# Performance work log

Hardware: AMD Instinct MI355X
Metric: run time of the kernel (lower is better)

## Reference

```python
import jax, jax.numpy as jnp
import numpy as np

B, S, D, H, V, N_SHARDS, CAP = 4, 512, 512, 8, 32000, 64, 128
HD = D // H


def _layernorm(x, g, b, eps=1e-5):
    mu = x.mean(-1, keepdims=True)
    var = ((x - mu) ** 2).mean(-1, keepdims=True)
    return (x - mu) * jax.lax.rsqrt(var + eps) * g + b


def setup_inputs() -> dict:
    key = jax.random.key(0)
    ks = jax.random.split(key, 16)
    s = 0.02
    return {
        'input_ids': jax.random.randint(ks[0], (B, S), 0, V, dtype=jnp.int32),
        'emb': jax.random.normal(ks[1], (V, D), jnp.float32) * s,
        'Wq': jax.random.normal(ks[2], (D, D), jnp.float32) * s,
        'Wk': jax.random.normal(ks[3], (D, D), jnp.float32) * s,
        'Wv': jax.random.normal(ks[4], (D, D), jnp.float32) * s,
        'Wo': jax.random.normal(ks[5], (D, D), jnp.float32) * s,
        'ln_g': jnp.ones((D,), jnp.float32),
        'ln_b': jnp.zeros((D,), jnp.float32),
        'W_router': jax.random.normal(ks[6], (D, N_SHARDS), jnp.float32),
        'mem_keys': jax.random.normal(ks[7], (N_SHARDS, CAP, D), jnp.float32) * s,
        'mem_values': jax.random.normal(ks[8], (N_SHARDS, CAP, D), jnp.float32) * s,
        'Wg_c': jax.random.normal(ks[9], (D, D), jnp.float32) * s,
        'Wg_m': jax.random.normal(ks[10], (D, D), jnp.float32) * s,
        'bg': jnp.zeros((D,), jnp.float32),
        'Wd': jax.random.normal(ks[11], (D, V), jnp.float32) * s,
        'bd': jnp.zeros((V,), jnp.float32),
        'top_k': 4,
    }


def reference(input_ids, emb, Wq, Wk, Wv, Wo, ln_g, ln_b, W_router,
              mem_keys, mem_values, Wg_c, Wg_m, bg, Wd, bd, top_k):
    # --- encode_context: embedding + causal MHA block (ContextSynthesizer) ---
    x = emb[input_ids]                                   # [B,S,D]
    q = (x @ Wq).reshape(B, S, H, HD)
    k = (x @ Wk).reshape(B, S, H, HD)
    v = (x @ Wv).reshape(B, S, H, HD)
    att = jnp.einsum('bqhd,bkhd->bhqk', q, k) / jnp.sqrt(jnp.float32(HD))
    causal = jnp.tril(jnp.ones((S, S), bool))
    att = jnp.where(causal[None, None], att, jnp.finfo(att.dtype).min)
    att = jax.nn.softmax(att, axis=-1)
    o = jnp.einsum('bhqk,bkhd->bqhd', att, v).reshape(B, S, D) @ Wo
    ctx = _layernorm(x + o, ln_g, ln_b)                  # [B,S,D]

    # --- LSHRouter: hyperplane projection -> shard id per token ---
    routes = jnp.argmax(ctx @ W_router, axis=-1)         # [B,S] int

    # --- MemoryShardStore.query, batched: per-token routed shard top-k read ---
    keys_g = mem_keys[routes]                            # [B,S,CAP,D] irregular gather
    scores = jnp.einsum('bscd,bsd->bsc', keys_g, ctx)    # [B,S,CAP]
    top_v, top_i = jax.lax.top_k(scores, top_k)          # [B,S,k]
    w = jax.nn.softmax(top_v, axis=-1)
    vals = mem_values[routes[:, :, None], top_i]         # [B,S,k,D]
    memory_stream = jnp.einsum('bsk,bskd->bsd', w, vals)

    # --- GatedMemoryFusion ---
    gate = jax.nn.sigmoid(ctx @ Wg_c + memory_stream @ Wg_m + bg)
    fused = gate * ctx + (1.0 - gate) * memory_stream

    # --- decoder; payload bias is zero (store holds no sequence_chunk records) ---
    logits = fused @ Wd + bd                             # [B,S,V]
    return logits
```

## Files before the change

### kernel.cpp

```cpp
#include <hip/hip_runtime.h>

typedef unsigned short u16;
typedef float f32x4 __attribute__((ext_vector_type(4)));
typedef short short8 __attribute__((ext_vector_type(8)));
typedef __bf16 bf16x8 __attribute__((ext_vector_type(8)));

#define B_  4
#define S_  512
#define D_  512
#define H_  8
#define HD_ 64
#define V_  32000
#define NSHARD_ 64
#define CAP_ 128
#define TOK_ (B_ * S_)

__device__ __forceinline__ float bf2f(u16 u) { return __uint_as_float(((unsigned)u) << 16); }
__device__ __forceinline__ u16 f2bf(float f) {
  unsigned u = __float_as_uint(f);
  u += 0x7FFFu + ((u >> 16) & 1u);
  return (u16)(u >> 16);
}

__device__ __forceinline__ f32x4 mfma16(short8 a, short8 b, f32x4 c) {
  return __builtin_amdgcn_mfma_f32_16x16x32_bf16(
      __builtin_bit_cast(bf16x8, a), __builtin_bit_cast(bf16x8, b), c, 0, 0, 0);
}

__device__ __forceinline__ void load_lds16(const void* g, void* l) {
  __builtin_amdgcn_global_load_lds(
      (const __attribute__((address_space(1))) void*)g,
      (__attribute__((address_space(3))) void*)l, 16, 0, 0);
}

template<int NS, bool ACC, int OM, bool CKLIM>
__global__ __launch_bounds__(256) void gemm_bt(
    const u16* __restrict__ Ah, const u16* __restrict__ Al, int ldA, long sA1, long sA2,
    const u16* __restrict__ Bh, const u16* __restrict__ Bl, int ldB, long sB1, long sB2,
    void* __restrict__ C0, void* __restrict__ C1, int ldC, long sC1, long sC2,
    int K, int z2n, float alpha)
{
  __shared__ u16 AsH[64 * 64];
  __shared__ u16 BsH[64 * 64];
  __shared__ u16 AsL[(NS == 3) ? 64 * 64 : 8];
  __shared__ u16 BsL[(NS == 3) ? 64 * 64 : 8];

  const int n0 = blockIdx.x * 64;
  const int m0 = blockIdx.y * 64;

  const int z = blockIdx.z;
  const int z1 = z / z2n, z2 = z - z1 * z2n;
  const long baseA = (long)z1 * sA1 + (long)z2 * sA2;
  const long baseB = (long)z1 * sB1 + (long)z2 * sB2;
  const long baseC = (long)z1 * sC1 + (long)z2 * sC2;

  const int tid = threadIdx.x;
  const int lane = tid & 63;
  const int w = tid >> 6;
  const int wm = (w >> 1) * 32, wn = (w & 1) * 32;
  const int fr = lane & 15, kg = lane >> 4;

  const int srow = lane >> 3;
  const int schunk = (lane & 7) ^ srow;

  const u16* gAh = Ah + baseA + (long)(m0 + w * 16 + srow) * ldA + schunk * 8;
  const u16* gBh = Bh + baseB + (long)(n0 + w * 16 + srow) * ldB + schunk * 8;
  const u16* gAl = (NS == 3) ? (Al + baseA + (long)(m0 + w * 16 + srow) * ldA + schunk * 8) : nullptr;
  const u16* gBl = (NS == 3) ? (Bl + baseB + (long)(n0 + w * 16 + srow) * ldB + schunk * 8) : nullptr;
  u16* lAh = &AsH[(w * 16) * 64];
  u16* lBh = &BsH[(w * 16) * 64];
  u16* lAl = &AsL[(NS == 3) ? (w * 16) * 64 : 0];
  u16* lBl = &BsL[(NS == 3) ? (w * 16) * 64 : 0];

  const int kmax = CKLIM ? (m0 + 64) : K;

  f32x4 acc[2][2] = {};

  for (int k0 = 0; k0 < kmax; k0 += 64) {
    load_lds16(gAh + k0, lAh);
    load_lds16(gAh + k0 + 8 * ldA, lAh + 8 * 64);
    load_lds16(gBh + k0, lBh);
    load_lds16(gBh + k0 + 8 * ldB, lBh + 8 * 64);
    if (NS == 3) {
      load_lds16(gAl + k0, lAl);
      load_lds16(gAl + k0 + 8 * ldA, lAl + 8 * 64);
      load_lds16(gBl + k0, lBl);
      load_lds16(gBl + k0 + 8 * ldB, lBl + 8 * 64);
    }
    __syncthreads();

    short8 ah[2][2], bh[2][2], al[2][2], bl[2][2];
#pragma unroll
    for (int mi = 0; mi < 2; ++mi) {
      int row = wm + mi * 16 + fr;
#pragma unroll
      for (int ks = 0; ks < 2; ++ks) {
        int idx = row * 64 + ((ks * 32 + kg * 8) ^ ((fr & 7) << 3));
        ah[mi][ks] = *(const short8*)&AsH[idx];
        if (NS == 3) al[mi][ks] = *(const short8*)&AsL[idx];
      }
    }
#pragma unroll
    for (int ni = 0; ni < 2; ++ni) {
      int row = wn + ni * 16 + fr;
#pragma unroll
      for (int ks = 0; ks < 2; ++ks) {
        int idx = row * 64 + ((ks * 32 + kg * 8) ^ ((fr & 7) << 3));
        bh[ni][ks] = *(const short8*)&BsH[idx];
        if (NS == 3) bl[ni][ks] = *(const short8*)&BsL[idx];
      }
    }
#pragma unroll
    for (int ks = 0; ks < 2; ++ks)
#pragma unroll
      for (int mi = 0; mi < 2; ++mi)
#pragma unroll
        for (int ni = 0; ni < 2; ++ni) {
          acc[mi][ni] = mfma16(ah[mi][ks], bh[ni][ks], acc[mi][ni]);
          if (NS == 3) {
            acc[mi][ni] = mfma16(ah[mi][ks], bl[ni][ks], acc[mi][ni]);
            acc[mi][ni] = mfma16(al[mi][ks], bh[ni][ks], acc[mi][ni]);
          }
        }
    __syncthreads();
  }

#pragma unroll
  for (int mi = 0; mi < 2; ++mi)
#pragma unroll
    for (int ni = 0; ni < 2; ++ni) {
      int gnc = n0 + wn + ni * 16 + fr;
#pragma unroll
      for (int r = 0; r < 4; ++r) {
        int gm = m0 + wm + mi * 16 + kg * 4 + r;
        float v = acc[mi][ni][r] * alpha;
        long idx = baseC + (long)gm * ldC + gnc;
        if (OM == 0) {
          float* C = (float*)C0;
          C[idx] = ACC ? (C[idx] + v) : v;
        } else {
          u16 h = f2bf(v);
          ((u16*)C0)[idx] = h;
          ((u16*)C1)[idx] = f2bf(v - bf2f(h));
        }
      }
    }
}

__global__ __launch_bounds__(256) void qkt_k(
    const u16* __restrict__ qkvh, const u16* __restrict__ qkvl,
    float* __restrict__ att)
{
  const int n0 = blockIdx.x * 64;
  const int m0 = blockIdx.y * 64;
  if (n0 > m0 + 63) return;
  const int z = blockIdx.z;
  const int b = z >> 3, h = z & 7;
  const long qbase = (long)b * 512 * 1536 + h * 64;
  const long kbase = qbase + 512;
  const long cbase = (long)z * 512 * 512;

  const int tid = threadIdx.x;
  const int lane = tid & 63;
  const int w = tid >> 6;
  const int wm = (w >> 1) * 32, wn = (w & 1) * 32;
  const int fr = lane & 15, kg = lane >> 4;

  short8 ah[2][2], al[2][2], bh[2][2], bl[2][2];
#pragma unroll
  for (int mi = 0; mi < 2; ++mi)
#pragma unroll
    for (int ks = 0; ks < 2; ++ks) {
      long ra = qbase + (long)(m0 + wm + mi * 16 + fr) * 1536 + ks * 32 + kg * 8;
      ah[mi][ks] = *(const short8*)(qkvh + ra);
      al[mi][ks] = *(const short8*)(qkvl + ra);
    }
#pragma unroll
  for (int ni = 0; ni < 2; ++ni)
#pragma unroll
    for (int ks = 0; ks < 2; ++ks) {
      long rb = kbase + (long)(n0 + wn + ni * 16 + fr) * 1536 + ks * 32 + kg * 8;
      bh[ni][ks] = *(const short8*)(qkvh + rb);
      bl[ni][ks] = *(const short8*)(qkvl + rb);
    }

  f32x4 acc[2][2] = {};
#pragma unroll
  for (int ks = 0; ks < 2; ++ks)
#pragma unroll
    for (int mi = 0; mi < 2; ++mi)
#pragma unroll
      for (int ni = 0; ni < 2; ++ni) {
        acc[mi][ni] = mfma16(ah[mi][ks], bh[ni][ks], acc[mi][ni]);
        acc[mi][ni] = mfma16(ah[mi][ks], bl[ni][ks], acc[mi][ni]);
        acc[mi][ni] = mfma16(al[mi][ks], bh[ni][ks], acc[mi][ni]);
      }

#pragma unroll
  for (int mi = 0; mi < 2; ++mi)
#pragma unroll
    for (int ni = 0; ni < 2; ++ni) {
      int gnc = n0 + wn + ni * 16 + fr;
#pragma unroll
      for (int r = 0; r < 4; ++r) {
        int gm = m0 + wm + mi * 16 + kg * 4 + r;
        att[cbase + (long)gm * 512 + gnc] = acc[mi][ni][r] * 0.125f;
      }
    }
}

__global__ __launch_bounds__(512, 2) void logits_gemm256_k(
    const u16* __restrict__ A, const u16* __restrict__ Bt,
    const float* __restrict__ bias, float* __restrict__ C)
{
  __shared__ u16 As[2][256 * 64];
  __shared__ u16 Bs[2][256 * 64];

  const int id = blockIdx.x;
  const int swz = (id & 7) * 125 + (id >> 3);
  const int n0 = (swz >> 3) * 256;
  const int m0 = (swz & 7) * 256;

  const int tid = threadIdx.x;
  const int lane = tid & 63;
  const int wid = tid >> 6;
  const int wr = wid >> 2, wc = wid & 3;
  const int fr = lane & 15, kg = lane >> 4;
  const int srow = lane >> 3;
  const int schunk = (lane & 7) ^ srow;

  f32x4 acc[8][4] = {};
  short8 pa0[4][2], pa1[4][2], pb0[2][2], pb1[2][2];

  auto stageA = [&](int kt, int h) {
#pragma unroll
    for (int j = 0; j < 2; ++j) {
      int r0 = j * 128 + h * 64 + wid * 8;
      load_lds16(A + (long)(m0 + r0 + srow) * D_ + kt * 64 + schunk * 8,
                 &As[kt & 1][r0 * 64]);
    }
  };
  auto stageB = [&](int kt, int h) {
#pragma unroll
    for (int j = 0; j < 2; ++j) {
      int r0 = (j * 2 + (wid >> 2)) * 64 + h * 32 + (wid & 3) * 8;
      load_lds16(Bt + (long)(n0 + r0 + srow) * D_ + kt * 64 + schunk * 8,
                 &Bs[kt & 1][r0 * 64]);
    }
  };
  auto readA = [&](short8 (&d)[4][2], int buf, int h) {
#pragma unroll
    for (int mi = 0; mi < 4; ++mi)
#pragma unroll
      for (int ks = 0; ks < 2; ++ks) {
        int row = wr * 128 + h * 64 + mi * 16 + fr;
        d[mi][ks] = *(const short8*)&As[buf][row * 64 +
                        ((ks * 32 + kg * 8) ^ ((fr & 7) << 3))];
      }
  };
  auto readB = [&](short8 (&d)[2][2], int buf, int h) {
#pragma unroll
    for (int ni = 0; ni < 2; ++ni)
#pragma unroll
      for (int ks = 0; ks < 2; ++ks) {
        int row = wc * 64 + h * 32 + ni * 16 + fr;
        d[ni][ks] = *(const short8*)&Bs[buf][row * 64 +
                        ((ks * 32 + kg * 8) ^ ((fr & 7) << 3))];
      }
  };
  auto quad = [&](short8 (&a)[4][2], short8 (&b)[2][2], int mb, int nb) {
#pragma unroll
    for (int ks = 0; ks < 2; ++ks)
#pragma unroll
      for (int mi = 0; mi < 4; ++mi)
#pragma unroll
        for (int ni = 0; ni < 2; ++ni)
          acc[mb + mi][nb + ni] = mfma16(a[mi][ks], b[ni][ks], acc[mb + mi][nb + ni]);
  };

#define SYNC_PRE()                                          \
  __builtin_amdgcn_sched_barrier(0);                        \
  __builtin_amdgcn_s_barrier();                             \
  asm volatile("s_waitcnt lgkmcnt(0)" ::: "memory");        \
  __builtin_amdgcn_sched_barrier(0);                        \
  __builtin_amdgcn_s_setprio(1);
#define SYNC_POST()                                         \
  __builtin_amdgcn_s_setprio(0);                            \
  __builtin_amdgcn_sched_barrier(0);                        \
  __builtin_amdgcn_s_barrier();                             \
  __builtin_amdgcn_sched_barrier(0);

  stageA(0, 0); stageB(0, 0); stageB(0, 1); stageA(0, 1);
  stageA(1, 0); stageB(1, 0); stageB(1, 1);
  __builtin_amdgcn_sched_barrier(0);
  asm volatile("s_waitcnt vmcnt(6)" ::: "memory");
  __builtin_amdgcn_s_barrier();
  __builtin_amdgcn_sched_barrier(0);

  for (int i = 0; i < 4; ++i) {
    const int t1 = 2 * i + 1, t2 = 2 * i + 2, t3 = 2 * i + 3;
    const bool st2 = (t2 < 8), st3 = (t3 < 8);

    readA(pa0, 0, 0); readB(pb0, 0, 0);
    stageA(t1, 1);
    SYNC_PRE(); quad(pa0, pb0, 0, 0); SYNC_POST();

    readB(pb1, 0, 1);
    if (st2) stageA(t2, 0);
    SYNC_PRE(); quad(pa0, pb1, 0, 2); SYNC_POST();

    readA(pa1, 0, 1);
    if (st2) stageB(t2, 0);
    SYNC_PRE(); quad(pa1, pb1, 4, 2); SYNC_POST();

    if (st2) stageB(t2, 1);
    __builtin_amdgcn_sched_barrier(0);
    if (st2) { asm volatile("s_waitcnt vmcnt(6)" ::: "memory"); }
    else     { asm volatile("s_waitcnt vmcnt(0)" ::: "memory"); }
    __builtin_amdgcn_s_barrier();
    __builtin_amdgcn_sched_barrier(0);
    __builtin_amdgcn_s_setprio(1);
    quad(pa1, pb0, 4, 0);
    SYNC_POST();

    readA(pa0, 1, 0); readB(pb0, 1, 0);
    if (st2) stageA(t2, 1);
    SYNC_PRE(); quad(pa0, pb0, 0, 0); SYNC_POST();

    readB(pb1, 1, 1);
    if (st3) stageA(t3, 0);
    SYNC_PRE(); quad(pa0, pb1, 0, 2); SYNC_POST();

    readA(pa1, 1, 1);
    if (st3) stageB(t3, 0);
    SYNC_PRE(); quad(pa1, pb1, 4, 2); SYNC_POST();

    if (st3) stageB(t3, 1);
    __builtin_amdgcn_sched_barrier(0);
    if (st3) { asm volatile("s_waitcnt vmcnt(6)" ::: "memory"); }
    else     { asm volatile("s_waitcnt vmcnt(0)" ::: "memory"); }
    __builtin_amdgcn_s_barrier();
    __builtin_amdgcn_sched_barrier(0);
    __builtin_amdgcn_s_setprio(1);
    quad(pa1, pb0, 4, 0);
    SYNC_POST();
  }
#undef SYNC_PRE
#undef SYNC_POST

#pragma unroll
  for (int ni = 0; ni < 4; ++ni) {
    int gnc = n0 + wc * 64 + ni * 16 + fr;
    float bv = bias[gnc];
#pragma unroll
    for (int mi = 0; mi < 8; ++mi)
#pragma unroll
      for (int r = 0; r < 4; ++r) {
        int gm = m0 + wr * 128 + mi * 16 + kg * 4 + r;
        __builtin_nontemporal_store(acc[mi][ni][r] + bv, &C[(long)gm * V_ + gnc]);
      }
  }
}

template<bool LO>
__global__ __launch_bounds__(256) void transpose_split_k(
    const float* __restrict__ W, int ldw, int ldo, int koff,
    u16* __restrict__ oh, u16* __restrict__ ol)
{
  __shared__ float t[64][65];
  const int n0 = blockIdx.x * 64;
  const int k0 = blockIdx.y * 64;
  const int tid = threadIdx.x;
  {
    const int kk = tid >> 4;
    const int c4 = (tid & 15) * 4;
#pragma unroll
    for (int i = 0; i < 4; ++i) {
      f32x4 v = *(const f32x4*)(W + (long)(k0 + kk + i * 16) * ldw + n0 + c4);
      t[kk + i * 16][c4] = v[0];
      t[kk + i * 16][c4 + 1] = v[1];
      t[kk + i * 16][c4 + 2] = v[2];
      t[kk + i * 16][c4 + 3] = v[3];
    }
  }
  __syncthreads();
  {
    const int chunk = tid & 7;
    const int nn = tid >> 3;
#pragma unroll
    for (int j = 0; j < 2; ++j) {
      int n = nn + j * 32;
      u16 hbuf[8], lbuf[8];
#pragma unroll
      for (int e = 0; e < 8; ++e) {
        float fv = t[chunk * 8 + e][n];
        u16 h = f2bf(fv);
        hbuf[e] = h;
        if (LO) lbuf[e] = f2bf(fv - bf2f(h));
      }
      long ob = (long)(n0 + n) * ldo + koff + k0 + chunk * 8;
      *(short8*)(oh + ob) = *(short8*)hbuf;
      if (LO) *(short8*)(ol + ob) = *(short8*)lbuf;
    }
  }
}

__global__ __launch_bounds__(256) void v_transpose_k(
    const u16* __restrict__ qh, const u16* __restrict__ ql,
    u16* __restrict__ vTh, u16* __restrict__ vTl)
{
  __shared__ u16 th[64][68];
  __shared__ u16 tl[64][68];
  const int z = blockIdx.y;
  const int b = z >> 3, h = z & 7;
  const int s0 = blockIdx.x * 64;
  const long ibase = ((long)(b * 512 + s0)) * 1536 + 1024 + h * 64;
  const int tid = threadIdx.x;
  {
    const int sr = tid >> 2;
    const int c8 = (tid & 3) * 16;
    const long src = ibase + (long)sr * 1536 + c8;
    *(short8*)&th[sr][c8]     = *(const short8*)(qh + src);
    *(short8*)&th[sr][c8 + 8] = *(const short8*)(qh + src + 8);
    *(short8*)&tl[sr][c8]     = *(const short8*)(ql + src);
    *(short8*)&tl[sr][c8 + 8] = *(const short8*)(ql + src + 8);
  }
  __syncthreads();
  {
    const int dr = tid >> 2;
    const int s8 = (tid & 3) * 16;
    u16 oh[16], ol[16];
#pragma unroll
    for (int j = 0; j < 16; ++j) { oh[j] = th[s8 + j][dr]; ol[j] = tl[s8 + j][dr]; }
    long ob = (long)z * 64 * 512 + (long)dr * 512 + s0 + s8;
    *(short8*)(vTh + ob)     = *(short8*)&oh[0];
    *(short8*)(vTh + ob + 8) = *(short8*)&oh[8];
    *(short8*)(vTl + ob)     = *(short8*)&ol[0];
    *(short8*)(vTl + ob + 8) = *(short8*)&ol[8];
  }
}

__global__ __launch_bounds__(128) void embed_k(const int* __restrict__ ids,
                                               const float* __restrict__ emb,
                                               float* __restrict__ x,
                                               u16* __restrict__ xh,
                                               u16* __restrict__ xl) {
  const int t = blockIdx.x;
  const long id = ids[t];
  const int c = threadIdx.x * 4;
  f32x4 v = *(const f32x4*)(emb + id * (long)D_ + c);
  *(f32x4*)(x + (long)t * D_ + c) = v;
  u16 hh[4], ll[4];
#pragma unroll
  for (int j = 0; j < 4; ++j) {
    u16 h = f2bf(v[j]);
    hh[j] = h;
    ll[j] = f2bf(v[j] - bf2f(h));
  }
  *(unsigned long long*)(xh + (long)t * D_ + c) = *(unsigned long long*)hh;
  *(unsigned long long*)(xl + (long)t * D_ + c) = *(unsigned long long*)ll;
}

__global__ __launch_bounds__(64) void softmax_causal_k(
    const float* __restrict__ att, u16* __restrict__ ph, u16* __restrict__ pl) {
  const int row = blockIdx.x;
  const int i = row & 511;
  const long base = (long)row << 9;
  const float* p = att + base;
  const int lane = threadIdx.x;
  const int c0 = lane * 8;
  float v[8];
  float m = -3.4e38f;
  if (c0 <= i) {
    f32x4 a = *(const f32x4*)(p + c0);
    f32x4 b2 = *(const f32x4*)(p + c0 + 4);
#pragma unroll
    for (int j = 0; j < 8; ++j) {
      float x = (j < 4) ? a[j] : b2[j - 4];
      x = (c0 + j <= i) ? x : -3.4e38f;
      v[j] = x;
      m = fmaxf(m, x);
    }
  } else {
#pragma unroll
    for (int j = 0; j < 8; ++j) v[j] = 0.f;
  }
#pragma unroll
  for (int off = 32; off; off >>= 1) m = fmaxf(m, __shfl_xor(m, off));
  float s = 0.f;
  if (c0 <= i) {
#pragma unroll
    for (int j = 0; j < 8; ++j) {
      float e = (c0 + j <= i) ? expf(v[j] - m) : 0.f;
      v[j] = e;
      s += e;
    }
  }
#pragma unroll
  for (int off = 32; off; off >>= 1) s += __shfl_xor(s, off);
  float inv = 1.f / s;
  if (c0 <= (i | 63)) {
    u16 hh[8], ll[8];
#pragma unroll
    for (int j = 0; j < 8; ++j) {
      float e = (c0 <= i) ? v[j] * inv : 0.f;
      u16 h = f2bf(e);
      hh[j] = h;
      ll[j] = f2bf(e - bf2f(h));
    }
    *(short8*)(ph + base + c0) = *(short8*)hh;
    *(short8*)(pl + base + c0) = *(short8*)ll;
  }
}

__global__ __launch_bounds__(256) void resid_ln_k(
    const float* __restrict__ x, const float* __restrict__ proj,
    const float* __restrict__ g, const float* __restrict__ b,
    float* __restrict__ ctxf, u16* __restrict__ catA)
{
  const int t = blockIdx.x;
  const int tid = threadIdx.x;
  __shared__ float red[8];
  const float* xr = x + (long)t * D_;
  const float* pr = proj + (long)t * D_;
  float v0 = xr[tid] + pr[tid];
  float v1 = xr[tid + 256] + pr[tid + 256];
  float s = v0 + v1, q = v0 * v0 + v1 * v1;
#pragma unroll
  for (int off = 32; off; off >>= 1) { s += __shfl_xor(s, off); q += __shfl_xor(q, off); }
  const int wave = tid >> 6, lane = tid & 63;
  if (lane == 0) { red[wave] = s; red[4 + wave] = q; }
  __syncthreads();
  s = red[0] + red[1] + red[2] + red[3];
  q = red[4] + red[5] + red[6] + red[7];
  float mu = s * (1.f / 512.f);
  float var = q * (1.f / 512.f) - mu * mu;
  float rs = rsqrtf(var + 1e-5f);
  float o0 = (v0 - mu) * rs * g[tid] + b[tid];
  float o1 = (v1 - mu) * rs * g[tid + 256] + b[tid + 256];
  long base = (long)t * D_;
  ctxf[base + tid] = o0;
  ctxf[base + tid + 256] = o1;
  long cb = (long)t * 1024;
  catA[cb + tid] = f2bf(o0);
  catA[cb + tid + 256] = f2bf(o1);
}

__global__ __launch_bounds__(128) void route_mem_k(
    const float* __restrict__ ctxf, const float* __restrict__ Wr,
    const float* __restrict__ keys, const float* __restrict__ valsm,
    float* __restrict__ msf, u16* __restrict__ catA)
{
  const int t = blockIdx.x;
  const int tid = threadIdx.x;
  __shared__ float sctx[D_];
  __shared__ float spart[CAP_];
  __shared__ float sred2[2][64];
  __shared__ int s_route;
  __shared__ int sidx[4];
  __shared__ float sw[4];

  f32x4 cv = ((const f32x4*)(ctxf + (long)t * D_))[tid];
  ((f32x4*)sctx)[tid] = cv;
  __syncthreads();

  {
    const int c = tid & 63, half = tid >> 6;
    float accr = 0.f;
    const float* cp = sctx + half * 256;
    const float* wp = Wr + (long)(half * 256) * NSHARD_ + c;
    for (int d = 0; d < 256; ++d) accr += cp[d] * wp[(long)d * NSHARD_];
    sred2[half][c] = accr;
  }
  __syncthreads();
  if (tid < 64) {
    float v = sred2[0][tid] + sred2[1][tid];
    int idx = tid;
#pragma unroll
    for (int off = 32; off; off >>= 1) {
      float ov = __shfl_xor(v, off);
      int oi = __shfl_xor(idx, off);
      if (ov > v || (ov == v && oi < idx)) { v = ov; idx = oi; }
    }
    if (tid == 0) s_route = idx;
  }
  __syncthreads();
  const int route = s_route;

  {
    const float* krow = keys + ((long)route * CAP_ + tid) * D_;
    float sc = 0.f;
    for (int d0 = 0; d0 < D_; d0 += 4) {
      f32x4 kv = *(const f32x4*)(krow + d0);
      sc += sctx[d0] * kv[0] + sctx[d0 + 1] * kv[1] +
            sctx[d0 + 2] * kv[2] + sctx[d0 + 3] * kv[3];
    }
    spart[tid] = sc;
  }
  __syncthreads();

  for (int rep = 0; rep < 4; ++rep) {
    if (tid < 64) {
      float v1 = spart[tid]; int i1 = tid;
      float v2 = spart[tid + 64]; int i2 = tid + 64;
      float v; int idx;
      if (v2 > v1) { v = v2; idx = i2; } else { v = v1; idx = i1; }
#pragma unroll
      for (int off = 32; off; off >>= 1) {
        float ov = __shfl_xor(v, off);
        int oi = __shfl_xor(idx, off);
        if (ov > v || (ov == v && oi < idx)) { v = ov; idx = oi; }
      }
      if (tid == 0) { sidx[rep] = idx; sw[rep] = v; spart[idx] = -3.4e38f; }
    }
    __syncthreads();
  }

  float w0 = sw[0], w1 = sw[1], w2 = sw[2], w3 = sw[3];
  float mx = fmaxf(fmaxf(w0, w1), fmaxf(w2, w3));
  float e0 = expf(w0 - mx), e1 = expf(w1 - mx), e2 = expf(w2 - mx), e3 = expf(w3 - mx);
  float inv = 1.f / (e0 + e1 + e2 + e3);
  float wk[4] = {e0 * inv, e1 * inv, e2 * inv, e3 * inv};

  float a0 = 0, a1 = 0, a2 = 0, a3 = 0;
#pragma unroll
  for (int k = 0; k < 4; ++k) {
    const float* vr = valsm + ((long)route * CAP_ + sidx[k]) * D_ + tid * 4;
    f32x4 vv = *(const f32x4*)vr;
    float w = wk[k];
    a0 += w * vv[0]; a1 += w * vv[1]; a2 += w * vv[2]; a3 += w * vv[3];
  }
  f32x4 of; of[0] = a0; of[1] = a1; of[2] = a2; of[3] = a3;
  *(f32x4*)(msf + (long)t * D_ + tid * 4) = of;
  u16 oh[4];
  oh[0] = f2bf(a0); oh[1] = f2bf(a1); oh[2] = f2bf(a2); oh[3] = f2bf(a3);
  *(unsigned long long*)(catA + (long)t * 1024 + 512 + tid * 4) =
      *(unsigned long long*)oh;
}

__global__ __launch_bounds__(256) void gate_fuse_k(
    const float* __restrict__ g1, const float* __restrict__ bg,
    const float* __restrict__ ctxf, const float* __restrict__ msf,
    u16* __restrict__ fused)
{
  long base = ((long)blockIdx.x * 256 + threadIdx.x) * 4;
  f32x4 gv = *(const f32x4*)(g1 + base);
  f32x4 cv = *(const f32x4*)(ctxf + base);
  f32x4 mv = *(const f32x4*)(msf + base);
  int col = (int)(base & 511);
  u16 o[4];
#pragma unroll
  for (int j = 0; j < 4; ++j) {
    float g = 1.f / (1.f + expf(-(gv[j] + bg[col + j])));
    o[j] = f2bf(g * cv[j] + (1.f - g) * mv[j]);
  }
  *(unsigned long long*)(fused + base) = *(unsigned long long*)o;
}

extern "C" void kernel_launch(void* const* d_in, const int* in_sizes, int n_in,
                              void* d_out, int out_size, void* d_ws, size_t ws_size,
                              hipStream_t stream) {
  const int*   ids  = (const int*)d_in[0];
  const float* emb  = (const float*)d_in[1];
  const float* Wq   = (const float*)d_in[2];
  const float* Wk   = (const float*)d_in[3];
  const float* Wv   = (const float*)d_in[4];
  const float* Wo   = (const float*)d_in[5];
  const float* ln_g = (const float*)d_in[6];
  const float* ln_b = (const float*)d_in[7];
  const float* Wr   = (const float*)d_in[8];
  const float* mk   = (const float*)d_in[9];
  const float* mv   = (const float*)d_in[10];
  const float* Wgc  = (const float*)d_in[11];
  const float* Wgm  = (const float*)d_in[12];
  const float* bg   = (const float*)d_in[13];
  const float* Wd   = (const float*)d_in[14];
  const float* bd   = (const float*)d_in[15];
  float* out = (float*)d_out;

  char* ws = (char*)d_ws;
  size_t off = 0;
  auto alloc = [&](size_t bytes) -> void* {
    void* p = ws + off;
    off += (bytes + 255) & ~(size_t)255;
    return p;
  };
  float* x      = (float*)alloc((size_t)TOK_ * D_ * 4);
  u16*   xh     = (u16*)  alloc((size_t)TOK_ * D_ * 2);
  u16*   xl     = (u16*)  alloc((size_t)TOK_ * D_ * 2);
  u16*   wqkvTh = (u16*)  alloc((size_t)3 * D_ * D_ * 2);
  u16*   wqkvTl = (u16*)  alloc((size_t)3 * D_ * D_ * 2);
  u16*   woTh   = (u16*)  alloc((size_t)D_ * D_ * 2);
  u16*   woTl   = (u16*)  alloc((size_t)D_ * D_ * 2);
  u16*   wgT    = (u16*)  alloc((size_t)D_ * 1024 * 2);
  u16*   wdT    = (u16*)  alloc((size_t)D_ * V_ * 2);
  u16*   qkvh   = (u16*)  alloc((size_t)TOK_ * 3 * D_ * 2);
  u16*   qkvl   = (u16*)  alloc((size_t)TOK_ * 3 * D_ * 2);
  u16*   vTh    = (u16*)  alloc((size_t)B_ * H_ * HD_ * S_ * 2);
  u16*   vTl    = (u16*)  alloc((size_t)B_ * H_ * HD_ * S_ * 2);
  float* att    = (float*)alloc((size_t)B_ * H_ * S_ * S_ * 4);
  u16*   ph     = (u16*)  alloc((size_t)B_ * H_ * S_ * S_ * 2);
  u16*   pl     = (u16*)  alloc((size_t)B_ * H_ * S_ * S_ * 2);
  u16*   oh     = (u16*)  alloc((size_t)TOK_ * D_ * 2);
  u16*   ol     = (u16*)  alloc((size_t)TOK_ * D_ * 2);
  float* proj   = (float*)alloc((size_t)TOK_ * D_ * 4);
  float* ctxf   = (float*)alloc((size_t)TOK_ * D_ * 4);
  u16*   catA   = (u16*)  alloc((size_t)TOK_ * 1024 * 2);
  float* msf    = (float*)alloc((size_t)TOK_ * D_ * 4);
  float* g1     = (float*)alloc((size_t)TOK_ * D_ * 4);
  u16*   fused  = (u16*)  alloc((size_t)TOK_ * D_ * 2);

  {
    dim3 g8(D_ / 64, D_ / 64, 1);
    transpose_split_k<true><<<g8, 256, 0, stream>>>(Wq, D_, 512, 0, wqkvTh, wqkvTl);
    transpose_split_k<true><<<g8, 256, 0, stream>>>(Wk, D_, 512, 0, wqkvTh + D_ * D_, wqkvTl + D_ * D_);
    transpose_split_k<true><<<g8, 256, 0, stream>>>(Wv, D_, 512, 0, wqkvTh + 2 * D_ * D_, wqkvTl + 2 * D_ * D_);
    transpose_split_k<true><<<g8, 256, 0, stream>>>(Wo, D_, 512, 0, woTh, woTl);
    transpose_split_k<false><<<g8, 256, 0, stream>>>(Wgc, D_, 1024, 0, wgT, nullptr);
    transpose_split_k<false><<<g8, 256, 0, stream>>>(Wgm, D_, 1024, 512, wgT, nullptr);
    dim3 gd(V_ / 64, D_ / 64, 1);
    transpose_split_k<false><<<gd, 256, 0, stream>>>(Wd, V_, 512, 0, wdT, nullptr);
  }

  embed_k<<<TOK_, 128, 0, stream>>>(ids, emb, x, xh, xl);

  {
    dim3 g(1536 / 64, TOK_ / 64, 1);
    gemm_bt<3, false, 1, false><<<g, 256, 0, stream>>>(
        xh, xl, D_, 0, 0, wqkvTh, wqkvTl, D_, 0, 0,
        qkvh, qkvl, 1536, 0, 0, D_, 1, 1.f);
  }

  {
    dim3 g(S_ / 64, B_ * H_, 1);
    v_transpose_k<<<g, 256, 0, stream>>>(qkvh, qkvl, vTh, vTl);
  }

  {
    dim3 g(S_ / 64, S_ / 64, B_ * H_);
    qkt_k<<<g, 256, 0, stream>>>(qkvh, qkvl, att);
  }

  softmax_causal_k<<<B_ * H_ * S_, 64, 0, stream>>>(att, ph, pl);

  {
    dim3 g(1, S_ / 64, B_ * H_);
    gemm_bt<3, false, 1, true><<<g, 256, 0, stream>>>(
        ph, pl, S_, (long)H_ * S_ * S_, (long)S_ * S_,
        vTh, vTl, S_, (long)H_ * HD_ * S_, (long)HD_ * S_,
        oh, ol, D_, (long)S_ * D_, HD_,
        S_, H_, 1.f);
  }

  {
    dim3 g(D_ / 64, TOK_ / 64, 1);
    gemm_bt<3, false, 0, false><<<g, 256, 0, stream>>>(
        oh, ol, D_, 0, 0, woTh, woTl, D_, 0, 0,
        proj, nullptr, D_, 0, 0, D_, 1, 1.f);
  }

  resid_ln_k<<<TOK_, 256, 0, stream>>>(x, proj, ln_g, ln_b, ctxf, catA);

  route_mem_k<<<TOK_, 128, 0, stream>>>(ctxf, Wr, mk, mv, msf, catA);

  {
    dim3 g(D_ / 64, TOK_ / 64, 1);
    gemm_bt<1, false, 0, false><<<g, 256, 0, stream>>>(
        catA, nullptr, 1024, 0, 0, wgT, nullptr, 1024, 0, 0,
        g1, nullptr, D_, 0, 0, 1024, 1, 1.f);
  }

  gate_fuse_k<<<(TOK_ * D_) / (256 * 4), 256, 0, stream>>>(g1, bg, ctxf, msf, fused);

  logits_gemm256_k<<<1000, 512, 0, stream>>>(fused, wdT, bd, out);
}
```

Measured before the change: 322.1 us.

## Rewrite logits GEMM with 256x128 tiles, BK=32 and simpler double buffering

Replaces the 256x256-tile, BK=64 logits GEMM and its fine-grained quad-interleaved schedule with a 256x128 tile over 16 K-steps of 32. Each step loads all fragments and issues a 4x4 MFMA block. The grid doubles to 2000 blocks, and the smaller LDS and register footprint targets 4 blocks per CU for more occupancy and more tiles to fill the CUs. In exchange it loses operand reuse per tile, adds more barriers per K, and drops the overlap of LDS reads with MFMA.

Measured after the change: 322.4 us. No clear change (+0.1%).

```diff
diff --git a/kernel.cpp b/kernel.cpp
--- a/kernel.cpp
+++ b/kernel.cpp
@@ -209,154 +209,91 @@
     }
 }
 
-__global__ __launch_bounds__(512, 2) void logits_gemm256_k(
+__global__ __launch_bounds__(512, 4) void logits_gemm_bk32_k(
     const u16* __restrict__ A, const u16* __restrict__ Bt,
     const float* __restrict__ bias, float* __restrict__ C)
 {
-  __shared__ u16 As[2][256 * 64];
-  __shared__ u16 Bs[2][256 * 64];
+  __shared__ u16 As[2][256 * 32];
+  __shared__ u16 Bs[2][128 * 32];
 
   const int id = blockIdx.x;
-  const int swz = (id & 7) * 125 + (id >> 3);
-  const int n0 = (swz >> 3) * 256;
+  const int swz = (id & 7) * 250 + (id >> 3);
   const int m0 = (swz & 7) * 256;
+  const int n0 = (swz >> 3) * 128;
 
   const int tid = threadIdx.x;
   const int lane = tid & 63;
   const int wid = tid >> 6;
-  const int wr = wid >> 2, wc = wid & 3;
+  const int wr = wid >> 1;
+  const int wc = wid & 1;
   const int fr = lane & 15, kg = lane >> 4;
-  const int srow = lane >> 3;
-  const int schunk = (lane & 7) ^ srow;
-
-  f32x4 acc[8][4] = {};
-  short8 pa0[4][2], pa1[4][2], pb0[2][2], pb1[2][2];
-
-  auto stageA = [&](int kt, int h) {
-#pragma unroll
-    for (int j = 0; j < 2; ++j) {
-      int r0 = j * 128 + h * 64 + wid * 8;
-      load_lds16(A + (long)(m0 + r0 + srow) * D_ + kt * 64 + schunk * 8,
-                 &As[kt & 1][r0 * 64]);
-    }
+  const int srow = lane >> 2;
+  const int schunk = (lane & 3) ^ (srow & 3);
+
+  f32x4 acc[4][4] = {};
+  short8 a[4], b[4];
+
+  auto stage = [&](int kt) {
+    const int buf = kt & 1;
+    const long kc = (long)kt * 32 + schunk * 8;
+    load_lds16(A + (long)(m0 + wid * 16 + srow) * D_ + kc,
+               &As[buf][(wid * 16) * 32]);
+    load_lds16(A + (long)(m0 + 128 + wid * 16 + srow) * D_ + kc,
+               &As[buf][(128 + wid * 16) * 32]);
+    load_lds16(Bt + (long)(n0 + wid * 16 + srow) * D_ + kc,
+               &Bs[buf][(wid * 16) * 32]);
   };
-  auto stageB = [&](int kt, int h) {
-#pragma unroll
-    for (int j = 0; j < 2; ++j) {
-      int r0 = (j * 2 + (wid >> 2)) * 64 + h * 32 + (wid & 3) * 8;
-      load_lds16(Bt + (long)(n0 + r0 + srow) * D_ + kt * 64 + schunk * 8,
-                 &Bs[kt & 1][r0 * 64]);
+  auto readfrags = [&](int buf) {
+#pragma unroll
+    for (int mi = 0; mi < 4; ++mi) {
+      int row = wr * 64 + mi * 16 + fr;
+      a[mi] = *(const short8*)&As[buf][row * 32 + ((kg ^ (row & 3)) * 8)];
+    }
+#pragma unroll
+    for (int ni = 0; ni < 4; ++ni) {
+      int row = wc * 64 + ni * 16 + fr;
+      b[ni] = *(const short8*)&Bs[buf][row * 32 + ((kg ^ (row & 3)) * 8)];
     }
   };
-  auto readA = [&](short8 (&d)[4][2], int buf, int h) {
-#pragma unroll
-    for (int mi = 0; mi < 4; ++mi)
-#pragma unroll
-      for (int ks = 0; ks < 2; ++ks) {
-        int row = wr * 128 + h * 64 + mi * 16 + fr;
-        d[mi][ks] = *(const short8*)&As[buf][row * 64 +
-                        ((ks * 32 + kg * 8) ^ ((fr & 7) << 3))];
-      }
-  };
-  auto readB = [&](short8 (&d)[2][2], int buf, int h) {
-#pragma unroll
-    for (int ni = 0; ni < 2; ++ni)
-#pragma unroll
-      for (int ks = 0; ks < 2; ++ks) {
-        int row = wc * 64 + h * 32 + ni * 16 + fr;
-        d[ni][ks] = *(const short8*)&Bs[buf][row * 64 +
-                        ((ks * 32 + kg * 8) ^ ((fr & 7) << 3))];
-      }
-  };
-  auto quad = [&](short8 (&a)[4][2], short8 (&b)[2][2], int mb, int nb) {
-#pragma unroll
-    for (int ks = 0; ks < 2; ++ks)
-#pragma unroll
-      for (int mi = 0; mi < 4; ++mi)
-#pragma unroll
-        for (int ni = 0; ni < 2; ++ni)
-          acc[mb + mi][nb + ni] = mfma16(a[mi][ks], b[ni][ks], acc[mb + mi][nb + ni]);
-  };
-
-#define SYNC_PRE()                                          \
-  __builtin_amdgcn_sched_barrier(0);                        \
-  __builtin_amdgcn_s_barrier();                             \
-  asm volatile("s_waitcnt lgkmcnt(0)" ::: "memory");        \
-  __builtin_amdgcn_sched_barrier(0);                        \
-  __builtin_amdgcn_s_setprio(1);
-#define SYNC_POST()                                         \
-  __builtin_amdgcn_s_setprio(0);                            \
-  __builtin_amdgcn_sched_barrier(0);                        \
-  __builtin_amdgcn_s_barrier();                             \
-  __builtin_amdgcn_sched_barrier(0);
-
-  stageA(0, 0); stageB(0, 0); stageB(0, 1); stageA(0, 1);
-  stageA(1, 0); stageB(1, 0); stageB(1, 1);
-  __builtin_amdgcn_sched_barrier(0);
-  asm volatile("s_waitcnt vmcnt(6)" ::: "memory");
-  __builtin_amdgcn_s_barrier();
-  __builtin_amdgcn_sched_barrier(0);
-
-  for (int i = 0; i < 4; ++i) {
-    const int t1 = 2 * i + 1, t2 = 2 * i + 2, t3 = 2 * i + 3;
-    const bool st2 = (t2 < 8), st3 = (t3 < 8);
-
-    readA(pa0, 0, 0); readB(pb0, 0, 0);
-    stageA(t1, 1);
-    SYNC_PRE(); quad(pa0, pb0, 0, 0); SYNC_POST();
-
-    readB(pb1, 0, 1);
-    if (st2) stageA(t2, 0);
-    SYNC_PRE(); quad(pa0, pb1, 0, 2); SYNC_POST();
-
-    readA(pa1, 0, 1);
-    if (st2) stageB(t2, 0);
-    SYNC_PRE(); quad(pa1, pb1, 4, 2); SYNC_POST();
-
-    if (st2) stageB(t2, 1);
+
+  stage(0);
+  stage(1);
+
+  for (int t = 0; t < 16; ++t) {
     __builtin_amdgcn_sched_barrier(0);
-    if (st2) { asm volatile("s_waitcnt vmcnt(6)" ::: "memory"); }
-    else     { asm volatile("s_waitcnt vmcnt(0)" ::: "memory"); }
+    if (t < 15) { asm volatile("s_waitcnt vmcnt(3)" ::: "memory"); }
+    else        { asm volatile("s_waitcnt vmcnt(0)" ::: "memory"); }
     __builtin_amdgcn_s_barrier();
     __builtin_amdgcn_sched_barrier(0);
-    __builtin_amdgcn_s_setprio(1);
-    quad(pa1, pb0, 4, 0);
-    SYNC_POST();
-
-    readA(pa0, 1, 0); readB(pb0, 1, 0);
-    if (st2) stageA(t2, 1);
-    SYNC_PRE(); quad(pa0, pb0, 0, 0); SYNC_POST();
-
-    readB(pb1, 1, 1);
-    if (st3) stageA(t3, 0);
-    SYNC_PRE(); quad(pa0, pb1, 0, 2); SYNC_POST();
-
-    readA(pa1, 1, 1);
-    if (st3) stageB(t3, 0);
-    SYNC_PRE(); quad(pa1, pb1, 4, 2); SYNC_POST();
-
-    if (st3) stageB(t3, 1);
+
+    readfrags(t & 1);
+    asm volatile("s_waitcnt lgkmcnt(0)" ::: "memory");
     __builtin_amdgcn_sched_barrier(0);
-    if (st3) { asm volatile("s_waitcnt vmcnt(6)" ::: "memory"); }
-    else     { asm volatile("s_waitcnt vmcnt(0)" ::: "memory"); }
     __builtin_amdgcn_s_barrier();
     __builtin_amdgcn_sched_barrier(0);
+
+    if (t + 2 < 16) stage(t + 2);
+
+    __builtin_amdgcn_sched_barrier(0);
     __builtin_amdgcn_s_setprio(1);
-    quad(pa1, pb0, 4, 0);
-    SYNC_POST();
-  }
-#undef SYNC_PRE
-#undef SYNC_POST
+#pragma unroll
+    for (int mi = 0; mi < 4; ++mi)
+#pragma unroll
+      for (int ni = 0; ni < 4; ++ni)
+        acc[mi][ni] = mfma16(a[mi], b[ni], acc[mi][ni]);
+    __builtin_amdgcn_s_setprio(0);
+    __builtin_amdgcn_sched_barrier(0);
+  }
 
 #pragma unroll
   for (int ni = 0; ni < 4; ++ni) {
     int gnc = n0 + wc * 64 + ni * 16 + fr;
     float bv = bias[gnc];
 #pragma unroll
-    for (int mi = 0; mi < 8; ++mi)
+    for (int mi = 0; mi < 4; ++mi)
 #pragma unroll
       for (int r = 0; r < 4; ++r) {
-        int gm = m0 + wr * 128 + mi * 16 + kg * 4 + r;
+        int gm = m0 + wr * 64 + mi * 16 + kg * 4 + r;
         __builtin_nontemporal_store(acc[mi][ni][r] + bv, &C[(long)gm * V_ + gnc]);
       }
   }
@@ -772,5 +709,5 @@
 
   gate_fuse_k<<<(TOK_ * D_) / (256 * 4), 256, 0, stream>>>(g1, bg, ctxf, msf, fused);
 
-  logits_gemm256_k<<<1000, 512, 0, stream>>>(fused, wdT, bd, out);
-}
+  logits_gemm_bk32_k<<<2000, 512, 0, stream>>>(fused, wdT, bd, out);
+}
```
